# Kernel optimization log

Measured on AMD Instinct MI355X. Metric: run time of the kernel, lower is better.

The kernel has to match this reference:

```python
import jax, jax.numpy as jnp
import numpy as np

MESH = 128
ALPHA, KL, KS = 0.2, 0.3, 1.0

# 8 trilinear (CIC) corner offsets, shape (8, 3)
_OFFSETS = jnp.array([[i, j, k] for i in (0, 1) for j in (0, 1) for k in (0, 1)], dtype=jnp.int32)


def _cic_corners_weights(pos, mesh):
    """pos: [N,3] in grid units -> corners [N,8,3] int32, weights [N,8]."""
    i0 = jnp.floor(pos)
    frac = pos - i0                                    # [N,3]
    i0 = i0.astype(jnp.int32)
    corners = (i0[:, None, :] + _OFFSETS[None]) % mesh  # periodic wrap, [N,8,3]
    w = jnp.where(_OFFSETS[None] == 1, frac[:, None, :], 1.0 - frac[:, None, :])
    return corners, w.prod(-1)                          # [N,8,3], [N,8]


def cic_paint(pos, mesh):
    """Particle-to-mesh scatter (CIC deposit) onto a mesh^3 grid."""
    corners, w = _cic_corners_weights(pos, mesh)
    grid = jnp.zeros((mesh, mesh, mesh), dtype=pos.dtype)
    return grid.at[corners[..., 0], corners[..., 1], corners[..., 2]].add(w)


def cic_read(grid, pos):
    """Mesh-to-particle gather (CIC interpolation). grid: [M,M,M] -> [N]."""
    mesh = grid.shape[0]
    corners, w = _cic_corners_weights(pos, mesh)
    vals = grid[corners[..., 0], corners[..., 1], corners[..., 2]]  # [N,8]
    return (vals * w).sum(-1)


def fftk(mesh):
    """Angular wavenumber vectors broadcastable to the mesh^3 grid."""
    k = (2.0 * jnp.pi * jnp.fft.fftfreq(mesh)).astype(jnp.float32)
    return [k.reshape(mesh, 1, 1), k.reshape(1, mesh, 1), k.reshape(1, 1, mesh)]


def setup_inputs() -> dict:
    key = jax.random.key(0)
    k1, k2 = jax.random.split(key)
    n = MESH ** 3
    pos = jax.random.uniform(k1, (n, 3), dtype=jnp.float32) * MESH  # grid units
    vel = jax.random.normal(k2, (n, 3), dtype=jnp.float32)
    return {"pos": pos, "vel": vel, "full_drift_factor": jnp.ones((), dtype=jnp.float32)}


def reference(pos, vel, full_drift_factor):
    # 1. CIC paint -> density mesh
    delta = cic_paint(pos, MESH)
    # 2. 3D FFT
    delta_k = jnp.fft.fftn(delta)
    kvec = fftk(MESH)
    kk = kvec[0] ** 2 + kvec[1] ** 2 + kvec[2] ** 2
    kk_safe = jnp.where(kk == 0, 1.0, kk)
    # 3. PGD band-pass filter (zeroed at k=0)
    kl2, ks4 = KL ** 2, KS ** 4
    pgd_range = jnp.exp(-kl2 / kk_safe) * jnp.exp(-(kk ** 2) / ks4)
    pgd_range = jnp.where(kk == 0, 0.0, pgd_range)
    # inverse Laplacian kernel: -1/k^2, zero at k=0
    inv_lap = -jnp.where(kk == 0, 0.0, 1.0 / kk_safe)
    pot_k = delta_k * inv_lap * pgd_range
    # 4. three gradient IFFTs + CIC read-out at particle positions
    forces = jnp.stack(
        [cic_read(jnp.fft.ifftn(-1j * kvec[i] * pot_k).real.astype(pos.dtype), pos) for i in range(3)],
        axis=-1,
    )  # [N,3]
    v_pgd = (forces * ALPHA) / full_drift_factor
    vel_boosted = vel + v_pgd
    return (pos, vel_boosted)
```

## Files before the change

kernel.cpp:

```cpp
#include <hip/hip_runtime.h>

#define MESH  128
#define MESH2 16384
#define MESH3 2097152
#define NPART MESH3
#define TILE  16
#define LDP   (TILE + 1)
#define LDP2  129
#define CAP   6
#define BSTRIDE 1536
typedef unsigned int u32;
typedef unsigned short u16;
typedef unsigned long long u64;

__device__ __forceinline__ float2 cmul(float2 a, float2 b) {
    return make_float2(a.x * b.x - a.y * b.y, a.x * b.y + a.y * b.x);
}
__device__ __forceinline__ float2 cadd(float2 a, float2 b) {
    return make_float2(a.x + b.x, a.y + b.y);
}
__device__ __forceinline__ float2 csub(float2 a, float2 b) {
    return make_float2(a.x - b.x, a.y - b.y);
}
__device__ __forceinline__ u16 f2bf(float x) {
    u32 b = __float_as_uint(x);
    return (u16)((b + 0x7FFFu + ((b >> 16) & 1u)) >> 16);
}
__device__ __forceinline__ float bf2f(u16 h) {
    return __uint_as_float(((u32)h) << 16);
}

__device__ __forceinline__ void fft128_fwd_lds(float2 (*__restrict__ s)[LDP],
                                               const float2* __restrict__ tw,
                                               int l, int bb) {
    #pragma unroll
    for (int pr = 0; pr < 3; ++pr) {
        const int st = 2 * pr;
        const int logq = 5 - st;
        const int q = 1 << logq;
        const int j = bb & (q - 1);
        const int g = bb >> logq;
        const int i0 = (g << (logq + 2)) + j;
        const float2 x0 = s[i0][l], x1 = s[i0 + q][l];
        const float2 x2 = s[i0 + 2 * q][l], x3 = s[i0 + 3 * q][l];
        const int m = j << st;
        const float2 wA = tw[m], wA2 = tw[m + 32], wB = tw[2 * m];
        const float2 u0 = cadd(x0, x2), u2 = cmul(csub(x0, x2), wA);
        const float2 u1 = cadd(x1, x3), u3 = cmul(csub(x1, x3), wA2);
        s[i0][l]         = cadd(u0, u1);
        s[i0 + q][l]     = cmul(csub(u0, u1), wB);
        s[i0 + 2 * q][l] = cadd(u2, u3);
        s[i0 + 3 * q][l] = cmul(csub(u2, u3), wB);
        __syncthreads();
    }
    #pragma unroll
    for (int itn = 0; itn < 2; ++itn) {
        const int i0 = (bb + (itn << 5)) << 1;
        const float2 x0 = s[i0][l], x1 = s[i0 + 1][l];
        s[i0][l]     = cadd(x0, x1);
        s[i0 + 1][l] = csub(x0, x1);
    }
}

__device__ __forceinline__ void fft128_inv_lds_dual(float2 (*__restrict__ SA)[LDP],
                                                    float2 (*__restrict__ SB)[LDP],
                                                    const float2* __restrict__ tw,
                                                    int l, int bb) {
    #pragma unroll
    for (int pr = 0; pr < 3; ++pr) {
        const int st = 2 * pr;
        const int p = 1 << st;
        const int j = bb & (p - 1);
        const int g = bb >> st;
        const int i0 = (g << (st + 2)) + j;
        const float2 wA = tw[j << (6 - st)];
        const int mB = j << (5 - st);
        const float2 wB = tw[mB], wB2 = tw[mB + 32];
        {
            const float2 x0 = SA[i0][l], x1 = SA[i0 + p][l];
            const float2 x2 = SA[i0 + 2 * p][l], x3 = SA[i0 + 3 * p][l];
            const float2 a1 = cmul(x1, wA), a3 = cmul(x3, wA);
            const float2 u0 = cadd(x0, a1), u1 = csub(x0, a1);
            const float2 u2 = cadd(x2, a3), u3 = csub(x2, a3);
            const float2 b2 = cmul(u2, wB), b3 = cmul(u3, wB2);
            SA[i0][l]         = cadd(u0, b2);
            SA[i0 + p][l]     = cadd(u1, b3);
            SA[i0 + 2 * p][l] = csub(u0, b2);
            SA[i0 + 3 * p][l] = csub(u1, b3);
        }
        {
            const float2 x0 = SB[i0][l], x1 = SB[i0 + p][l];
            const float2 x2 = SB[i0 + 2 * p][l], x3 = SB[i0 + 3 * p][l];
            const float2 a1 = cmul(x1, wA), a3 = cmul(x3, wA);
            const float2 u0 = cadd(x0, a1), u1 = csub(x0, a1);
            const float2 u2 = cadd(x2, a3), u3 = csub(x2, a3);
            const float2 b2 = cmul(u2, wB), b3 = cmul(u3, wB2);
            SB[i0][l]         = cadd(u0, b2);
            SB[i0 + p][l]     = cadd(u1, b3);
            SB[i0 + 2 * p][l] = csub(u0, b2);
            SB[i0 + 3 * p][l] = csub(u1, b3);
        }
        __syncthreads();
    }
    #pragma unroll
    for (int itn = 0; itn < 2; ++itn) {
        const int b = bb + (itn << 5);
        const float2 w = tw[b];
        {
            const float2 u = SA[b][l];
            const float2 v = cmul(SA[b + 64][l], w);
            SA[b][l]      = cadd(u, v);
            SA[b + 64][l] = csub(u, v);
        }
        {
            const float2 u = SB[b][l];
            const float2 v = cmul(SB[b + 64][l], w);
            SB[b][l]      = cadd(u, v);
            SB[b + 64][l] = csub(u, v);
        }
    }
}

__global__ __launch_bounds__(512) void fft_y_fwd(float2* __restrict__ data) {
    __shared__ float2 s[MESH][LDP];
    __shared__ float2 tw[64];
    const int t = threadIdx.x;
    if (t < 64) {
        float sv, cv;
        sincospif(-(float)t / 64.0f, &sv, &cv);
        tw[t] = make_float2(cv, sv);
    }
    const int outer = blockIdx.x >> 3;
    const int z0 = (blockIdx.x & 7) * TILE;
    const int base = outer * MESH2 + z0;
    for (int i = t; i < MESH * TILE; i += 512) {
        const int l = i & 15, e = i >> 4;
        s[e][l] = data[base + e * MESH + l];
    }
    __syncthreads();
    const int l  = t & 15;
    const int bb = t >> 4;
    fft128_fwd_lds(s, tw, l, bb);
    __syncthreads();
    for (int i = t; i < MESH * TILE; i += 512) {
        const int l2 = i & 15, e = i >> 4;
        data[base + e * MESH + l2] = s[e][l2];
    }
}

__global__ __launch_bounds__(512) void fft_z_fwd_merge(const float* __restrict__ ST,
                                                       float2* __restrict__ out) {
    __shared__ float2 s[MESH][LDP];
    __shared__ float2 tw[64];
    const int t = threadIdx.x;
    if (t < 64) {
        float sv, cv;
        sincospif(-(float)t / 64.0f, &sv, &cv);
        tw[t] = make_float2(cv, sv);
    }
    const int col0 = blockIdx.x * TILE;
    const int base = col0 * MESH;
    for (int i = t; i < MESH * TILE; i += 512) {
        const int lc = i >> 7;
        const int z  = i & 127;
        const int c  = col0 + lc;
        const int x = c >> 7, y = c & 127;
        const int tx = x >> 2, ty = y >> 1;
        const int hx = x & 3,  hy = y & 1;
        float v = ST[((tx << 6) | ty) * 1920 + ((hx * 3 + hy) << 7) + z];
        const int txm = (tx + 31) & 31;
        const int tym = (ty + 63) & 63;
        if (hx == 0)
            v += ST[((txm << 6) | ty) * 1920 + ((12 + hy) << 7) + z];
        if (hy == 0) {
            v += ST[((tx << 6) | tym) * 1920 + ((hx * 3 + 2) << 7) + z];
            if (hx == 0)
                v += ST[((txm << 6) | tym) * 1920 + (14 << 7) + z];
        }
        s[z][lc] = make_float2(v, 0.0f);
    }
    __syncthreads();
    const int l  = t & 15;
    const int bb = t >> 4;
    fft128_fwd_lds(s, tw, l, bb);
    __syncthreads();
    for (int i = t; i < MESH * TILE; i += 512)
        out[base + i] = s[i & 127][i >> 7];
}

__global__ __launch_bounds__(1024) void fft_yz_inv_mega(const float2* __restrict__ A,
                                                        const float2* __restrict__ B,
                                                        u32* __restrict__ Abf,
                                                        u16* __restrict__ Brl) {
    __shared__ float2 s[MESH][LDP2];
    __shared__ float2 tw[64];
    const int t = threadIdx.x;
    if (t < 64) {
        float sv, cv;
        sincospif(-(float)t / 64.0f, &sv, &cv);
        tw[t] = make_float2(cv, -sv);
    }
    const bool isB = blockIdx.x >= 128;
    const int x = blockIdx.x & 127;
    const float2* __restrict__ in = isB ? B : A;
    const int gbase = x * MESH2;
    for (int i = t; i < MESH * MESH; i += 1024)
        s[i >> 7][i & 127] = in[gbase + i];
    __syncthreads();

    const int col = t & 127;
    const int wrk = t >> 7;

    #pragma unroll
    for (int pr = 0; pr < 3; ++pr) {
        const int st = 2 * pr;
        const int p = 1 << st;
        #pragma unroll
        for (int n = 0; n < 4; ++n) {
            const int bb = wrk | (n << 3);
            const int j = bb & (p - 1);
            const int g = bb >> st;
            const int i0 = (g << (st + 2)) + j;
            const float2 wA = tw[j << (6 - st)];
            const int mB = j << (5 - st);
            const float2 wB = tw[mB], wB2 = tw[mB + 32];
            const float2 x0 = s[i0][col], x1 = s[i0 + p][col];
            const float2 x2 = s[i0 + 2 * p][col], x3 = s[i0 + 3 * p][col];
            const float2 a1 = cmul(x1, wA), a3 = cmul(x3, wA);
            const float2 u0 = cadd(x0, a1), u1 = csub(x0, a1);
            const float2 u2 = cadd(x2, a3), u3 = csub(x2, a3);
            const float2 b2 = cmul(u2, wB), b3 = cmul(u3, wB2);
            s[i0][col]         = cadd(u0, b2);
            s[i0 + p][col]     = cadd(u1, b3);
            s[i0 + 2 * p][col] = csub(u0, b2);
            s[i0 + 3 * p][col] = csub(u1, b3);
        }
        __syncthreads();
    }
    #pragma unroll
    for (int n = 0; n < 8; ++n) {
        const int b = wrk | (n << 3);
        const float2 w = tw[b];
        const float2 u = s[b][col];
        const float2 v = cmul(s[b + 64][col], w);
        s[b][col]      = cadd(u, v);
        s[b + 64][col] = csub(u, v);
    }
    __syncthreads();

    const int row = t & 127;
    #pragma unroll
    for (int pr = 0; pr < 3; ++pr) {
        const int st = 2 * pr;
        const int p = 1 << st;
        #pragma unroll
        for (int n = 0; n < 4; ++n) {
            const int bb = wrk | (n << 3);
            const int j = bb & (p - 1);
            const int g = bb >> st;
            const int i0 = (g << (st + 2)) + j;
            const float2 wA = tw[j << (6 - st)];
            const int mB = j << (5 - st);
            const float2 wB = tw[mB], wB2 = tw[mB + 32];
            const float2 x0 = s[row][i0], x1 = s[row][i0 + p];
            const float2 x2 = s[row][i0 + 2 * p], x3 = s[row][i0 + 3 * p];
            const float2 a1 = cmul(x1, wA), a3 = cmul(x3, wA);
            const float2 u0 = cadd(x0, a1), u1 = csub(x0, a1);
            const float2 u2 = cadd(x2, a3), u3 = csub(x2, a3);
            const float2 b2 = cmul(u2, wB), b3 = cmul(u3, wB2);
            s[row][i0]         = cadd(u0, b2);
            s[row][i0 + p]     = cadd(u1, b3);
            s[row][i0 + 2 * p] = csub(u0, b2);
            s[row][i0 + 3 * p] = csub(u1, b3);
        }
        __syncthreads();
    }
    #pragma unroll
    for (int n = 0; n < 8; ++n) {
        const int b = wrk | (n << 3);
        const float2 w = tw[b];
        const float2 u = s[row][b];
        const float2 v = cmul(s[row][b + 64], w);
        s[row][b]      = cadd(u, v);
        s[row][b + 64] = csub(u, v);
    }
    __syncthreads();

    if (isB) {
        for (int i = t; i < MESH * MESH; i += 1024)
            Brl[gbase + i] = f2bf(s[i >> 7][i & 127].x);
    } else {
        for (int i = t; i < MESH * MESH; i += 1024) {
            const float2 v = s[i >> 7][i & 127];
            Abf[gbase + i] = (u32)f2bf(v.x) | ((u32)f2bf(v.y) << 16);
        }
    }
}

__global__ __launch_bounds__(512) void fft_x_mega(float2* __restrict__ A,
                                                  float2* __restrict__ B) {
    __shared__ float2 SA[MESH][LDP];
    __shared__ float2 SB[MESH][LDP];
    __shared__ float2 twf[64];
    __shared__ float2 twi[64];
    const int t = threadIdx.x;
    if (t < 64) {
        float sv, cv;
        sincospif(-(float)t / 64.0f, &sv, &cv);
        twf[t] = make_float2(cv, sv);
        twi[t] = make_float2(cv, -sv);
    }
    const int cy = blockIdx.x >> 3;
    const int z0 = (blockIdx.x & 7) * TILE;
    const int base = cy * MESH + z0;

    for (int i = t; i < MESH * TILE; i += 512) {
        const int l = i & 15, e = i >> 4;
        SA[e][l] = A[base + e * MESH2 + l];
    }
    __syncthreads();

    const int l  = t & 15;
    const int bb = t >> 4;
    fft128_fwd_lds(SA, twf, l, bb);
    __syncthreads();

    const int jy = (int)(__brev((unsigned)cy) >> 25);
    const float c = 6.28318530717958647692f / 128.0f;
    const float ky = c * (float)(jy < 64 ? jy : jy - 128);
    for (int i = t; i < MESH * TILE; i += 512) {
        const int e = i & 127, ll = i >> 7;
        const int jx = (int)(__brev((unsigned)e) >> 25);
        const int jz = (int)(__brev((unsigned)(z0 + ll)) >> 25);
        const float kx = c * (float)(jx < 64 ? jx : jx - 128);
        const float kz = c * (float)(jz < 64 ? jz : jz - 128);
        const float kk = kx * kx + ky * ky + kz * kz;
        float2 a = SA[e][ll];
        float2 av = make_float2(0.f, 0.f), bv = make_float2(0.f, 0.f);
        if (kk > 0.0f) {
            const float inv_kk = 1.0f / kk;
            const float rng = __expf(-0.09f * inv_kk - kk * kk);
            const float sc  = -inv_kk * rng * (1.0f / 2097152.0f);
            const float pr = a.x * sc, pi = a.y * sc;
            av = make_float2(ky * pr + kx * pi, ky * pi - kx * pr);
            bv = make_float2(kz * pi, -kz * pr);
        }
        SA[e][ll] = av;
        SB[e][ll] = bv;
    }
    __syncthreads();

    fft128_inv_lds_dual(SA, SB, twi, l, bb);
    __syncthreads();

    for (int i = t; i < MESH * TILE; i += 512) {
        const int l2 = i & 15, e = i >> 4;
        A[base + e * MESH2 + l2] = SA[e][l2];
        B[base + e * MESH2 + l2] = SB[e][l2];
    }
}


__device__ __forceinline__ int bucket_of(float px, float py) {
    const int ix = ((int)floorf(px)) & 127;
    const int iy = ((int)floorf(py)) & 127;
    return ((ix >> 2) << 6) | (iy >> 1);
}

__device__ __forceinline__ u64 make_rec(float px, float py, float pz, int n) {
    const float fxx = floorf(px), fyy = floorf(py), fzz = floorf(pz);
    const int ix = ((int)fxx) & 127, iy = ((int)fyy) & 127, iz = ((int)fzz) & 127;
    const u32 qx = (u32)((px - fxx) * 1024.0f);
    const u32 qy = (u32)((py - fyy) * 1024.0f);
    const u32 qz = (u32)((pz - fzz) * 1024.0f);
    return (u64)iz | ((u64)(ix & 3) << 7) | ((u64)(iy & 1) << 9)
         | ((u64)qx << 11) | ((u64)qy << 21) | ((u64)qz << 31)
         | ((u64)(u32)n << 41);
}

__global__ __launch_bounds__(1024) void bin_kernel(const float* __restrict__ pos,
                                                   u32* __restrict__ gcnt,
                                                   u64* __restrict__ S,
                                                   float4* __restrict__ outp) {
    __shared__ u32 h[2048];
    const int t = threadIdx.x;
    for (int i = t; i < 2048; i += 1024) h[i] = 0;
    __syncthreads();
    const float4* pos4 = (const float4*)pos;
    const int base_q = blockIdx.x * 2048;
    float4 P[2][3];
    #pragma unroll
    for (int it = 0; it < 2; ++it) {
        const int q = base_q + (it << 10) + t;
        const float4 Pa = pos4[3 * q], Pb = pos4[3 * q + 1], Pc = pos4[3 * q + 2];
        P[it][0] = Pa; P[it][1] = Pb; P[it][2] = Pc;
        outp[3 * q]     = Pa;
        outp[3 * q + 1] = Pb;
        outp[3 * q + 2] = Pc;
        atomicAdd(&h[bucket_of(Pa.x, Pa.y)], 1u);
        atomicAdd(&h[bucket_of(Pa.w, Pb.x)], 1u);
        atomicAdd(&h[bucket_of(Pb.z, Pb.w)], 1u);
        atomicAdd(&h[bucket_of(Pc.y, Pc.z)], 1u);
    }
    __syncthreads();
    for (int i = t; i < 2048; i += 1024) {
        const u32 c = h[i];
        h[i] = c ? ((u32)i * BSTRIDE + atomicAdd(&gcnt[i], c)) : 0u;
    }
    __syncthreads();
    #pragma unroll
    for (int it = 0; it < 2; ++it) {
        const int q = base_q + (it << 10) + t;
        const int n = 4 * q;
        const float4 Pa = P[it][0], Pb = P[it][1], Pc = P[it][2];
        S[atomicAdd(&h[bucket_of(Pa.x, Pa.y)], 1u)] = make_rec(Pa.x, Pa.y, Pa.z, n);
        S[atomicAdd(&h[bucket_of(Pa.w, Pb.x)], 1u)] = make_rec(Pa.w, Pb.x, Pb.y, n + 1);
        S[atomicAdd(&h[bucket_of(Pb.z, Pb.w)], 1u)] = make_rec(Pb.z, Pb.w, Pc.x, n + 2);
        S[atomicAdd(&h[bucket_of(Pc.y, Pc.z)], 1u)] = make_rec(Pc.y, Pc.z, Pc.w, n + 3);
    }
}

__device__ __forceinline__ void decode(u64 v, int& iz, int& lx, int& ly,
                                       float& fx, float& fy, float& fz, int& n) {
    iz = (int)(v & 127);
    lx = (int)((v >> 7) & 3);
    ly = (int)((v >> 9) & 3);
    const float inv = 1.0f / 1024.0f;
    fx = (float)((v >> 11) & 1023) * inv;
    fy = (float)((v >> 21) & 1023) * inv;
    fz = (float)((v >> 31) & 1023) * inv;
    n = (int)((v >> 41) & 0x1FFFFF);
}

__global__ __launch_bounds__(512) void paint_kernel(const u64* __restrict__ S,
                                                    const u32* __restrict__ gcnt,
                                                    float* __restrict__ ST) {
    __shared__ u32 cnt[1024];
    __shared__ u32 rec[1024 * CAP];
    __shared__ u64 ovf[128];
    __shared__ u32 novf;
    const int t = threadIdx.x;
    for (int i = t; i < 1024; i += 512) cnt[i] = 0;
    if (t == 0) novf = 0;
    __syncthreads();
    const int b = blockIdx.x;
    const int start = b * BSTRIDE;
    const int end = start + (int)gcnt[b];
    for (int i = start + t; i < end; i += 512) {
        const u64 v = S[i];
        const int iz = (int)(v & 127);
        const int lx = (int)((v >> 7) & 3);
        const int ly = (int)((v >> 9) & 1);
        const int cell = (((lx << 1) | ly) << 7) | iz;
        const u32 r = (u32)((v >> 11) & 0x3FFFFFFFull);
        const u32 slot = atomicAdd(&cnt[cell], 1u);
        if (slot < CAP) rec[cell * CAP + slot] = r;
        else {
            const u32 o = atomicAdd(&novf, 1u);
            if (o < 128u) ovf[o] = ((u64)cell << 32) | r;
        }
    }
    __syncthreads();
    const u32 nv = novf > 128u ? 128u : novf;
    const float inv = 1.0f / 1024.0f;
    for (int i = t; i < 1920; i += 512) {
        const int hx = i / 384;
        const int hy = (i >> 7) % 3;
        const int z  = i & 127;
        float acc = 0.0f;
        #pragma unroll
        for (int sx = 0; sx < 2; ++sx) {
            const int bx = hx - 1 + sx;
            if ((unsigned)bx > 3u) continue;
            #pragma unroll
            for (int sy = 0; sy < 2; ++sy) {
                const int by = hy - 1 + sy;
                if ((unsigned)by > 1u) continue;
                #pragma unroll
                for (int sz = 0; sz < 2; ++sz) {
                    const int bz = (z - 1 + sz) & 127;
                    const int c = (((bx << 1) | by) << 7) | bz;
                    const int m = (int)min(cnt[c], (u32)CAP);
                    const int rb = c * CAP;
                    for (int k = 0; k < m; ++k) {
                        const u32 r = rec[rb + k];
                        const float fx = (float)(r & 1023) * inv;
                        const float fy = (float)((r >> 10) & 1023) * inv;
                        const float fz = (float)(r >> 20) * inv;
                        const float wx = sx ? (1.0f - fx) : fx;
                        const float wy = sy ? (1.0f - fy) : fy;
                        const float wz = sz ? (1.0f - fz) : fz;
                        acc += wx * wy * wz;
                    }
                }
            }
        }
        for (u32 j = 0; j < nv; ++j) {
            const u64 o = ovf[j];
            const int c = (int)(o >> 32);
            const int obx = (c >> 8) & 3, oby = (c >> 7) & 1, obz = c & 127;
            const int dx = hx - obx, dy = hy - oby, dz = (z - obz) & 127;
            if ((unsigned)dx < 2u && (unsigned)dy < 2u && dz < 2) {
                const u32 r = (u32)o;
                const float fx = (float)(r & 1023) * inv;
                const float fy = (float)((r >> 10) & 1023) * inv;
                const float fz = (float)(r >> 20) * inv;
                acc += (dx ? fx : 1.0f - fx) * (dy ? fy : 1.0f - fy)
                     * (dz ? fz : 1.0f - fz);
            }
        }
        ST[(size_t)b * 1920 + i] = acc;
    }
}

__global__ __launch_bounds__(512) void force_kernel(const u64* __restrict__ S,
                                                    const u32* __restrict__ gcnt,
                                                    const u32* __restrict__ Abf,
                                                    const u16* __restrict__ Brl,
                                                    u64* __restrict__ VP) {
    __shared__ float2 sxy[1920];
    __shared__ float  szz[1920];
    const int t = threadIdx.x;
    const int b = blockIdx.x;
    const int x0 = (b >> 6) << 2, y0 = (b & 63) << 1;
    for (int i = t; i < 1920; i += 512) {
        const int hx = i / 384;
        const int hy = (i >> 7) % 3;
        const int z = i & 127;
        const int g = (((x0 + hx) & 127) << 14) | (((y0 + hy) & 127) << 7) | z;
        const u32 ab = Abf[g];
        sxy[i] = make_float2(__uint_as_float(ab << 16),
                             __uint_as_float(ab & 0xFFFF0000u));
        szz[i] = bf2f(Brl[g]);
    }
    __syncthreads();
    const int start = b * BSTRIDE;
    const int end = start + (int)gcnt[b];
    for (int i = start + t; i < end; i += 512) {
        int iz, lx, ly, n;
        float fx, fy, fz;
        decode(S[i], iz, lx, ly, fx, fy, fz, n);
        const float wx[2] = {1.0f - fx, fx};
        const float wy[2] = {1.0f - fy, fy};
        const float wz[2] = {1.0f - fz, fz};
        float gx = 0.f, gy = 0.f, gz = 0.f;
        #pragma unroll
        for (int dx = 0; dx < 2; ++dx)
            #pragma unroll
            for (int dy = 0; dy < 2; ++dy) {
                const int bi = ((lx + dx) * 3 + (ly + dy)) << 7;
                const float wxy = wx[dx] * wy[dy];
                #pragma unroll
                for (int dz = 0; dz < 2; ++dz) {
                    const int idx2 = bi + ((iz + dz) & 127);
                    const float w = wxy * wz[dz];
                    const float2 a = sxy[idx2];
                    gx += w * a.x;
                    gy += w * a.y;
                    gz += w * szz[idx2];
                }
            }
        VP[n] = (u64)f2bf(gx) | ((u64)f2bf(gy) << 16) | ((u64)f2bf(gz) << 32);
    }
}

__global__ __launch_bounds__(256) void finalize_kernel(const float* __restrict__ vel,
                                                       const u64* __restrict__ VP,
                                                       const float* __restrict__ fdf,
                                                       float* __restrict__ out) {
    const int tid = blockIdx.x * 256 + threadIdx.x;
    const float sc = 0.2f / fdf[0];
    const float4* vel4 = (const float4*)vel;
    float4* outv = (float4*)out + (3 * NPART / 4);
    const float4 Va = vel4[3 * tid], Vb = vel4[3 * tid + 1], Vc = vel4[3 * tid + 2];
    const ulonglong2* VP2 = (const ulonglong2*)VP;
    const ulonglong2 qa = VP2[2 * tid];
    const ulonglong2 qb = VP2[2 * tid + 1];
    const u64 q[4] = {qa.x, qa.y, qb.x, qb.y};
    const float vv[12] = {Va.x, Va.y, Va.z, Va.w, Vb.x, Vb.y, Vb.z, Vb.w,
                          Vc.x, Vc.y, Vc.z, Vc.w};
    float ov[12];
    #pragma unroll
    for (int k = 0; k < 4; ++k) {
        const float gx = bf2f((u16)(q[k] & 0xFFFF));
        const float gy = bf2f((u16)((q[k] >> 16) & 0xFFFF));
        const float gz = bf2f((u16)((q[k] >> 32) & 0xFFFF));
        ov[3 * k]     = vv[3 * k]     + gx * sc;
        ov[3 * k + 1] = vv[3 * k + 1] + gy * sc;
        ov[3 * k + 2] = vv[3 * k + 2] + gz * sc;
    }
    outv[3 * tid]     = make_float4(ov[0], ov[1], ov[2], ov[3]);
    outv[3 * tid + 1] = make_float4(ov[4], ov[5], ov[6], ov[7]);
    outv[3 * tid + 2] = make_float4(ov[8], ov[9], ov[10], ov[11]);
}

extern "C" void kernel_launch(void* const* d_in, const int* in_sizes, int n_in,
                              void* d_out, int out_size, void* d_ws, size_t ws_size,
                              hipStream_t stream) {
    const float* pos = (const float*)d_in[0];
    const float* vel = (const float*)d_in[1];
    const float* fdf = (const float*)d_in[2];
    float* out = (float*)d_out;

    char* w = (char*)d_ws;
    float2* A   = (float2*)(w);
    float2* B   = (float2*)(w + ((size_t)1 << 24));
    float*  ST  = (float*)(w + ((size_t)2 << 24));
    u32*    Abf = (u32*)(w + ((size_t)3 << 24));
    u16*    Brl = (u16*)(w + ((size_t)3 << 24) + (size_t)MESH3 * 4);
    u64*    VP  = (u64*)(w + ((size_t)4 << 24));
    u64*    S   = (u64*)(w + ((size_t)5 << 24));
    u32*    gcnt = (u32*)(w + ((size_t)7 << 24));

    hipMemsetAsync(gcnt, 0, 2048 * sizeof(u32), stream);
    bin_kernel<<<256, 1024, 0, stream>>>(pos, gcnt, S, (float4*)out);

    paint_kernel<<<2048, 512, 0, stream>>>(S, gcnt, ST);

    fft_z_fwd_merge<<<1024, 512, 0, stream>>>(ST, A);
    fft_y_fwd<<<1024, 512, 0, stream>>>(A);
    fft_x_mega<<<1024, 512, 0, stream>>>(A, B);
    fft_yz_inv_mega<<<256, 1024, 0, stream>>>(A, B, Abf, Brl);

    force_kernel<<<2048, 512, 0, stream>>>(S, gcnt, Abf, Brl, VP);
    finalize_kernel<<<2048, 256, 0, stream>>>(vel, VP, fdf, out);
}
```

Measured before the change: 249.3 us.

## Fuse forward z and y FFT passes into one per-plane kernel

Replaces the separate forward z-FFT (with tile merge) and y-FFT kernels with a single kernel where each block holds a full 128x128 yz plane in LDS and runs radix-4/radix-2 FFTs along z then y. This removes one full global round trip of the complex mesh and one kernel launch. In exchange the grid shrinks to 128 blocks of 1024 threads with a large LDS footprint, which may leave many CUs idle on a 256-CU device.

New measurement: 261.1 us. +4.7%, slower.

```diff
diff --git a/kernel.cpp b/kernel.cpp
--- a/kernel.cpp
+++ b/kernel.cpp
@@ -121,8 +121,9 @@
     }
 }
 
-__global__ __launch_bounds__(512) void fft_y_fwd(float2* __restrict__ data) {
-    __shared__ float2 s[MESH][LDP];
+__global__ __launch_bounds__(1024) void fft_zy_fwd_mega(const float* __restrict__ ST,
+                                                        float2* __restrict__ A) {
+    __shared__ float2 s[MESH][LDP2];
     __shared__ float2 tw[64];
     const int t = threadIdx.x;
     if (t < 64) {
@@ -130,45 +131,13 @@
         sincospif(-(float)t / 64.0f, &sv, &cv);
         tw[t] = make_float2(cv, sv);
     }
-    const int outer = blockIdx.x >> 3;
-    const int z0 = (blockIdx.x & 7) * TILE;
-    const int base = outer * MESH2 + z0;
-    for (int i = t; i < MESH * TILE; i += 512) {
-        const int l = i & 15, e = i >> 4;
-        s[e][l] = data[base + e * MESH + l];
-    }
-    __syncthreads();
-    const int l  = t & 15;
-    const int bb = t >> 4;
-    fft128_fwd_lds(s, tw, l, bb);
-    __syncthreads();
-    for (int i = t; i < MESH * TILE; i += 512) {
-        const int l2 = i & 15, e = i >> 4;
-        data[base + e * MESH + l2] = s[e][l2];
-    }
-}
-
-__global__ __launch_bounds__(512) void fft_z_fwd_merge(const float* __restrict__ ST,
-                                                       float2* __restrict__ out) {
-    __shared__ float2 s[MESH][LDP];
-    __shared__ float2 tw[64];
-    const int t = threadIdx.x;
-    if (t < 64) {
-        float sv, cv;
-        sincospif(-(float)t / 64.0f, &sv, &cv);
-        tw[t] = make_float2(cv, sv);
-    }
-    const int col0 = blockIdx.x * TILE;
-    const int base = col0 * MESH;
-    for (int i = t; i < MESH * TILE; i += 512) {
-        const int lc = i >> 7;
-        const int z  = i & 127;
-        const int c  = col0 + lc;
-        const int x = c >> 7, y = c & 127;
-        const int tx = x >> 2, ty = y >> 1;
-        const int hx = x & 3,  hy = y & 1;
+    const int x = blockIdx.x;
+    const int tx = x >> 2, hx = x & 3;
+    const int txm = (tx + 31) & 31;
+    for (int i = t; i < MESH * MESH; i += 1024) {
+        const int y = i >> 7, z = i & 127;
+        const int ty = y >> 1, hy = y & 1;
         float v = ST[((tx << 6) | ty) * 1920 + ((hx * 3 + hy) << 7) + z];
-        const int txm = (tx + 31) & 31;
         const int tym = (ty + 63) & 63;
         if (hx == 0)
             v += ST[((txm << 6) | ty) * 1920 + ((12 + hy) << 7) + z];
@@ -177,15 +146,82 @@
             if (hx == 0)
                 v += ST[((txm << 6) | tym) * 1920 + (14 << 7) + z];
         }
-        s[z][lc] = make_float2(v, 0.0f);
-    }
-    __syncthreads();
-    const int l  = t & 15;
-    const int bb = t >> 4;
-    fft128_fwd_lds(s, tw, l, bb);
-    __syncthreads();
-    for (int i = t; i < MESH * TILE; i += 512)
-        out[base + i] = s[i & 127][i >> 7];
+        s[y][z] = make_float2(v, 0.0f);
+    }
+    __syncthreads();
+
+    const int wrk = t >> 7;
+    const int row = t & 127;
+    #pragma unroll
+    for (int pr = 0; pr < 3; ++pr) {
+        const int st = 2 * pr;
+        const int logq = 5 - st;
+        const int q = 1 << logq;
+        #pragma unroll
+        for (int n = 0; n < 4; ++n) {
+            const int bb = wrk | (n << 3);
+            const int j = bb & (q - 1);
+            const int g = bb >> logq;
+            const int i0 = (g << (logq + 2)) + j;
+            const int m = j << st;
+            const float2 wA = tw[m], wA2 = tw[m + 32], wB = tw[2 * m];
+            const float2 x0 = s[row][i0], x1 = s[row][i0 + q];
+            const float2 x2 = s[row][i0 + 2 * q], x3 = s[row][i0 + 3 * q];
+            const float2 u0 = cadd(x0, x2), u2 = cmul(csub(x0, x2), wA);
+            const float2 u1 = cadd(x1, x3), u3 = cmul(csub(x1, x3), wA2);
+            s[row][i0]         = cadd(u0, u1);
+            s[row][i0 + q]     = cmul(csub(u0, u1), wB);
+            s[row][i0 + 2 * q] = cadd(u2, u3);
+            s[row][i0 + 3 * q] = cmul(csub(u2, u3), wB);
+        }
+        __syncthreads();
+    }
+    #pragma unroll
+    for (int n = 0; n < 8; ++n) {
+        const int i0 = (wrk | (n << 3)) << 1;
+        const float2 x0 = s[row][i0], x1 = s[row][i0 + 1];
+        s[row][i0]     = cadd(x0, x1);
+        s[row][i0 + 1] = csub(x0, x1);
+    }
+    __syncthreads();
+
+    const int col = t & 127;
+    #pragma unroll
+    for (int pr = 0; pr < 3; ++pr) {
+        const int st = 2 * pr;
+        const int logq = 5 - st;
+        const int q = 1 << logq;
+        #pragma unroll
+        for (int n = 0; n < 4; ++n) {
+            const int bb = wrk | (n << 3);
+            const int j = bb & (q - 1);
+            const int g = bb >> logq;
+            const int i0 = (g << (logq + 2)) + j;
+            const int m = j << st;
+            const float2 wA = tw[m], wA2 = tw[m + 32], wB = tw[2 * m];
+            const float2 x0 = s[i0][col], x1 = s[i0 + q][col];
+            const float2 x2 = s[i0 + 2 * q][col], x3 = s[i0 + 3 * q][col];
+            const float2 u0 = cadd(x0, x2), u2 = cmul(csub(x0, x2), wA);
+            const float2 u1 = cadd(x1, x3), u3 = cmul(csub(x1, x3), wA2);
+            s[i0][col]         = cadd(u0, u1);
+            s[i0 + q][col]     = cmul(csub(u0, u1), wB);
+            s[i0 + 2 * q][col] = cadd(u2, u3);
+            s[i0 + 3 * q][col] = cmul(csub(u2, u3), wB);
+        }
+        __syncthreads();
+    }
+    #pragma unroll
+    for (int n = 0; n < 8; ++n) {
+        const int i0 = (wrk | (n << 3)) << 1;
+        const float2 x0 = s[i0][col], x1 = s[i0 + 1][col];
+        s[i0][col]     = cadd(x0, x1);
+        s[i0 + 1][col] = csub(x0, x1);
+    }
+    __syncthreads();
+
+    const int gbase = x * MESH2;
+    for (int i = t; i < MESH * MESH; i += 1024)
+        A[gbase + i] = s[i >> 7][i & 127];
 }
 
 __global__ __launch_bounds__(1024) void fft_yz_inv_mega(const float2* __restrict__ A,
@@ -617,8 +653,7 @@
 
     paint_kernel<<<2048, 512, 0, stream>>>(S, gcnt, ST);
 
-    fft_z_fwd_merge<<<1024, 512, 0, stream>>>(ST, A);
-    fft_y_fwd<<<1024, 512, 0, stream>>>(A);
+    fft_zy_fwd_mega<<<128, 1024, 0, stream>>>(ST, A);
     fft_x_mega<<<1024, 512, 0, stream>>>(A, B);
     fft_yz_inv_mega<<<256, 1024, 0, stream>>>(A, B, Abf, Brl);
 
```
